# Kernel optimization log

Hardware: AMD Instinct MI355X
Metric: run time of the kernel (lower is better)

The kernel has to match this reference:

```python
import jax, jax.numpy as jnp
import numpy as np

B, S, I, H = 64, 512, 512, 1024

def setup_inputs() -> dict:
    key = jax.random.key(0)
    k1, k2, k3, k4, k5 = jax.random.split(key, 5)
    bound = 1.0 / np.sqrt(H)  # PyTorch RNNCell init scale (values only; distribution irrelevant for correctness)
    return {
        "x_in": jax.random.normal(k1, (B, S, I), dtype=jnp.float32),
        "W_ih": jax.random.uniform(k2, (H, I), dtype=jnp.float32, minval=-bound, maxval=bound),
        "W_hh": jax.random.uniform(k3, (H, H), dtype=jnp.float32, minval=-bound, maxval=bound),
        "b_ih": jax.random.uniform(k4, (H,), dtype=jnp.float32, minval=-bound, maxval=bound),
        "b_hh": jax.random.uniform(k5, (H,), dtype=jnp.float32, minval=-bound, maxval=bound),
    }

def reference(x_in, W_ih, W_hh, b_ih, b_hh):
    # batch_first=True: x_in is (B, S, I). Permute to time-major (S, B, I).
    x_tm = jnp.transpose(x_in, (1, 0, 2))
    # Precompute input projections for all timesteps in one big GEMM: (S, B, H)
    x_proj = jnp.einsum("sbi,hi->sbh", x_tm, W_ih) + b_ih + b_hh
    h0 = jnp.zeros((x_in.shape[0], W_hh.shape[0]), dtype=x_in.dtype)

    def step(h, xp_t):
        h_new = jnp.tanh(xp_t + h @ W_hh.T)
        return h_new, h_new

    _, hiddens = jax.lax.scan(step, h0, x_proj)  # (S, B, H)
    return jnp.transpose(hiddens, (1, 0, 2))  # back to (B, S, H)
```

## Files before the change

kernel.cpp:

```cpp
#include <hip/hip_runtime.h>
#include <hip/hip_bf16.h>
#include <math.h>

#define B_ 64
#define S_ 512
#define I_ 512
#define H_ 1024

typedef __attribute__((ext_vector_type(8))) short short8;
typedef __attribute__((ext_vector_type(4))) short short4v;
typedef __attribute__((ext_vector_type(4))) float f32x4;

__device__ inline short bf16bits(float f) {
    __hip_bfloat16 h = __float2bfloat16(f);
    return __builtin_bit_cast(short, h);
}

#define BM 128
#define BN 128
#define BK 32
#define LDT 40

__global__ __launch_bounds__(256) void xproj_gemm(const float* __restrict__ X,
                                                  const float* __restrict__ Wih,
                                                  const float* __restrict__ bih,
                                                  const float* __restrict__ bhh,
                                                  float* __restrict__ out) {
    __shared__ __hip_bfloat16 sA[BM * LDT];
    __shared__ __hip_bfloat16 sB[BN * LDT];
    const int tid  = threadIdx.x;
    const int m0   = blockIdx.x * BM;
    const int n0   = blockIdx.y * BN;
    const int wave = tid >> 6;
    const int lane = tid & 63;
    const int quad = lane >> 4;
    const int l16  = lane & 15;
    const int wm   = (wave >> 1) * 64;
    const int wn   = (wave & 1) * 64;

    f32x4 acc[4][4] = {};

    for (int k0 = 0; k0 < I_; k0 += BK) {
#pragma unroll
        for (int i = 0; i < 4; ++i) {
            int idx = tid + i * 256;
            int r   = idx >> 3;
            int c4  = idx & 7;
            f32x4 a = *reinterpret_cast<const f32x4*>(X   + (size_t)(m0 + r) * I_ + k0 + c4 * 4);
            f32x4 b = *reinterpret_cast<const f32x4*>(Wih + (size_t)(n0 + r) * I_ + k0 + c4 * 4);
            short4v ap, bp;
            ap[0] = bf16bits(a[0]); ap[1] = bf16bits(a[1]); ap[2] = bf16bits(a[2]); ap[3] = bf16bits(a[3]);
            bp[0] = bf16bits(b[0]); bp[1] = bf16bits(b[1]); bp[2] = bf16bits(b[2]); bp[3] = bf16bits(b[3]);
            int off = r * LDT + c4 * 4;
            *reinterpret_cast<short4v*>(&sA[off]) = ap;
            *reinterpret_cast<short4v*>(&sB[off]) = bp;
        }
        __syncthreads();

        short8 af[4], bf[4];
#pragma unroll
        for (int mt = 0; mt < 4; ++mt)
            af[mt] = *reinterpret_cast<const short8*>(&sA[(wm + mt * 16 + l16) * LDT + quad * 8]);
#pragma unroll
        for (int nt = 0; nt < 4; ++nt)
            bf[nt] = *reinterpret_cast<const short8*>(&sB[(wn + nt * 16 + l16) * LDT + quad * 8]);
#pragma unroll
        for (int mt = 0; mt < 4; ++mt)
#pragma unroll
            for (int nt = 0; nt < 4; ++nt)
                acc[mt][nt] = __builtin_amdgcn_mfma_f32_16x16x32_bf16(af[mt], bf[nt], acc[mt][nt], 0, 0, 0);
        __syncthreads();
    }

#pragma unroll
    for (int mt = 0; mt < 4; ++mt) {
#pragma unroll
        for (int nt = 0; nt < 4; ++nt) {
            int gm = m0 + wm + mt * 16 + quad * 4;
            int gn = n0 + wn + nt * 16 + l16;
            float bias = bih[gn] + bhh[gn];
#pragma unroll
            for (int r = 0; r < 4; ++r)
                out[(size_t)(gm + r) * H_ + gn] = acc[mt][nt][r] + bias;
        }
    }
}

#define WLD 1032

__global__ __launch_bounds__(256) void rnn_steps(const float* __restrict__ Whh,
                                                 float* __restrict__ out,
                                                 unsigned short* __restrict__ hbuf,
                                                 unsigned int* __restrict__ cnt) {
    __shared__ __hip_bfloat16 Wl[16 * WLD];
    __shared__ float red[4][16][17];
    const int tid  = threadIdx.x;
    const int bid  = blockIdx.x;
    const int g    = bid >> 6;
    const int jblk = bid & 63;
    const int j0   = jblk * 16;
    const int b0   = g * 16;
    const int wave = tid >> 6;
    const int lane = tid & 63;
    const int quad = lane >> 4;
    const int l16  = lane & 15;
    const int m    = tid >> 4;
    const int n    = tid & 15;

    for (int idx = tid; idx < 16 * 256; idx += 256) {
        int r  = idx >> 8;
        int c4 = idx & 255;
        f32x4 w = *reinterpret_cast<const f32x4*>(Whh + (size_t)(j0 + r) * H_ + c4 * 4);
        short4v wp;
        wp[0] = bf16bits(w[0]); wp[1] = bf16bits(w[1]); wp[2] = bf16bits(w[2]); wp[3] = bf16bits(w[3]);
        *reinterpret_cast<short4v*>(&Wl[r * WLD + c4 * 4]) = wp;
    }
    __syncthreads();

    const size_t orow = (size_t)(b0 + m) * S_ * H_ + (j0 + n);
    unsigned int* mycnt = cnt + g * 32;

    for (int t = 0; t < S_; ++t) {
        float xp = __builtin_nontemporal_load(out + orow + (size_t)t * H_);
        float s = 0.f;

        if (t > 0) {
            if (tid == 0) {
                const unsigned int target = (unsigned int)t * 64u;
                int guard = 0;
                while (__hip_atomic_load(mycnt, __ATOMIC_RELAXED, __HIP_MEMORY_SCOPE_AGENT) < target) {
                    __builtin_amdgcn_s_sleep(1);
                    if (++guard > 1000000) break;
                }
                (void)__hip_atomic_load(mycnt, __ATOMIC_ACQUIRE, __HIP_MEMORY_SCOPE_AGENT);
            }
            __syncthreads();

            const unsigned short* hprev = hbuf + (size_t)((t - 1) & 1) * (B_ * H_);
            f32x4 acc = {0.f, 0.f, 0.f, 0.f};
            const int kbase = wave * 256;
#pragma unroll
            for (int i = 0; i < 8; ++i) {
                int k = kbase + i * 32 + quad * 8;
                short8 av = *reinterpret_cast<const short8*>(hprev + (size_t)(b0 + l16) * H_ + k);
                short8 bv = *reinterpret_cast<const short8*>(&Wl[l16 * WLD + k]);
                acc = __builtin_amdgcn_mfma_f32_16x16x32_bf16(av, bv, acc, 0, 0, 0);
            }
#pragma unroll
            for (int r = 0; r < 4; ++r)
                red[wave][quad * 4 + r][l16] = acc[r];
            __syncthreads();

            s = red[0][m][n] + red[1][m][n] + red[2][m][n] + red[3][m][n];
        }

        float val = tanhf(xp + s);
        __builtin_nontemporal_store(val, out + orow + (size_t)t * H_);

        float nb = __shfl_xor(val, 1, 64);
        unsigned int pair = ((unsigned int)(unsigned short)bf16bits(nb) << 16)
                          | (unsigned int)(unsigned short)bf16bits(val);
        if ((n & 1) == 0) {
            unsigned int* dst = (unsigned int*)(hbuf + (size_t)(t & 1) * (B_ * H_)
                                                + (size_t)(b0 + m) * H_ + (j0 + n));
            __hip_atomic_store(dst, pair, __ATOMIC_RELAXED, __HIP_MEMORY_SCOPE_AGENT);
        }
        __syncthreads();

        if (t < S_ - 1 && tid == 0) {
            __hip_atomic_fetch_add(mycnt, 1u, __ATOMIC_RELAXED, __HIP_MEMORY_SCOPE_AGENT);
        }
    }
}

extern "C" void kernel_launch(void* const* d_in, const int* in_sizes, int n_in,
                              void* d_out, int out_size, void* d_ws, size_t ws_size,
                              hipStream_t stream) {
    const float* x   = (const float*)d_in[0];
    const float* Wih = (const float*)d_in[1];
    const float* Whh = (const float*)d_in[2];
    const float* bih = (const float*)d_in[3];
    const float* bhh = (const float*)d_in[4];
    float* out = (float*)d_out;

    unsigned int* cnt = (unsigned int*)d_ws;
    unsigned short* hbuf = (unsigned short*)((char*)d_ws + 1024);

    hipMemsetAsync(d_ws, 0, 1024, stream);

    dim3 gA(256, 8);
    xproj_gemm<<<gA, 256, 0, stream>>>(x, Wih, bih, bhh, out);
    rnn_steps<<<256, 256, 0, stream>>>(Whh, out, hbuf, cnt);
}
```

Baseline: 2.336 ms.

## Replace counter barrier with per-element step-tagged hidden state flags in RNN kernel

The recurrent kernel is restructured so each block owns 4 batch rows by 64 hidden units instead of 16 by 16. The shared atomic step counter and its barrier are replaced by tagging every stored hidden value with its timestep in the upper 16 bits. Consumers poll the exact hidden words they need with cache-bypassing loads until the tags match, which removes the global counter round-trip and one block-wide sync per step. The cost is twice the hidden-buffer size, a larger workspace requirement with a fallback path, wasted MFMA rows (only 4 of 16 batch rows are real), and spin polling on global memory.

```diff
diff --git a/kernel.cpp b/kernel.cpp
--- a/kernel.cpp
+++ b/kernel.cpp
@@ -10,6 +10,7 @@
 typedef __attribute__((ext_vector_type(8))) short short8;
 typedef __attribute__((ext_vector_type(4))) short short4v;
 typedef __attribute__((ext_vector_type(4))) float f32x4;
+typedef __attribute__((ext_vector_type(4))) unsigned int u32x4;
 
 __device__ inline short bf16bits(float f) {
     __hip_bfloat16 h = __float2bfloat16(f);
@@ -86,12 +87,128 @@
     }
 }
 
+#define WLD2 1032
+
+__global__ __launch_bounds__(256) void rnn_steps_v4(const float* __restrict__ Whh,
+                                                    float* __restrict__ out,
+                                                    unsigned int* __restrict__ hbuf) {
+    __shared__ __hip_bfloat16 Wl[64 * WLD2];
+    __shared__ float red[2][4][4][65];
+    const int tid  = threadIdx.x;
+    const int bid  = blockIdx.x;
+    const int g    = bid >> 4;
+    const int jblk = bid & 15;
+    const int j0   = jblk * 64;
+    const int b0   = g * 4;
+    const int wave = tid >> 6;
+    const int lane = tid & 63;
+    const int quad = lane >> 4;
+    const int l16  = lane & 15;
+    const int m    = wave;
+    const int n    = lane;
+
+    for (int idx = tid; idx < 64 * 256; idx += 256) {
+        int r  = idx >> 8;
+        int c4 = idx & 255;
+        f32x4 w = *reinterpret_cast<const f32x4*>(Whh + (size_t)(j0 + r) * H_ + c4 * 4);
+        short4v wp;
+        wp[0] = bf16bits(w[0]); wp[1] = bf16bits(w[1]); wp[2] = bf16bits(w[2]); wp[3] = bf16bits(w[3]);
+        *reinterpret_cast<short4v*>(&Wl[r * WLD2 + c4 * 4]) = wp;
+    }
+    __syncthreads();
+
+    const size_t orow = (size_t)(b0 + m) * S_ * H_ + (j0 + n);
+    const int rb = b0 + (l16 & 3);
+    const int kw = wave * 256 + quad * 8;
+    unsigned int* const hp0 = hbuf + (size_t)rb * H_ + kw;
+    unsigned int* const hp1 = hp0 + (size_t)(B_ * H_);
+    unsigned int* const hst = hbuf + (size_t)(b0 + m) * H_ + (j0 + n);
+
+    for (int t = 0; t < S_; ++t) {
+        float xp = __builtin_nontemporal_load(out + orow + (size_t)t * H_);
+        float s = 0.f;
+        const int par = t & 1;
+
+        if (t > 0) {
+            unsigned int* hp = ((t - 1) & 1) ? hp1 : hp0;
+            const unsigned int target = (unsigned int)t;
+            u32x4 wa[8], wb[8];
+
+#pragma unroll
+            for (int f = 0; f < 8; ++f)
+                asm volatile("global_load_dwordx4 %0, %2, off sc0 sc1\n\t"
+                             "global_load_dwordx4 %1, %2, off offset:16 sc0 sc1"
+                             : "=&v"(wa[f]), "=&v"(wb[f]) : "v"(hp + f * 32) : "memory");
+            asm volatile("s_waitcnt vmcnt(0)" ::: "memory");
+            __builtin_amdgcn_sched_barrier(0);
+
+            bool okf[8];
+            int sweep = 0;
+            while (true) {
+                bool allok = true;
+#pragma unroll
+                for (int f = 0; f < 8; ++f) {
+                    bool ok = ((wa[f][0] >> 16) == target) & ((wa[f][1] >> 16) == target)
+                            & ((wa[f][2] >> 16) == target) & ((wa[f][3] >> 16) == target)
+                            & ((wb[f][0] >> 16) == target) & ((wb[f][1] >> 16) == target)
+                            & ((wb[f][2] >> 16) == target) & ((wb[f][3] >> 16) == target);
+                    okf[f] = (bool)__all((int)ok);
+                    allok = allok && okf[f];
+                }
+                if (allok) break;
+                if (++sweep > 16384) break;
+                __builtin_amdgcn_s_sleep(1);
+#pragma unroll
+                for (int f = 0; f < 8; ++f)
+                    if (!okf[f])
+                        asm volatile("global_load_dwordx4 %0, %2, off sc0 sc1\n\t"
+                                     "global_load_dwordx4 %1, %2, off offset:16 sc0 sc1"
+                                     : "=&v"(wa[f]), "=&v"(wb[f]) : "v"(hp + f * 32) : "memory");
+                asm volatile("s_waitcnt vmcnt(0)" ::: "memory");
+                __builtin_amdgcn_sched_barrier(0);
+            }
+
+            f32x4 acc[4] = {};
+#pragma unroll
+            for (int f = 0; f < 8; ++f) {
+                short8 av;
+                av[0] = (short)wa[f][0]; av[1] = (short)wa[f][1];
+                av[2] = (short)wa[f][2]; av[3] = (short)wa[f][3];
+                av[4] = (short)wb[f][0]; av[5] = (short)wb[f][1];
+                av[6] = (short)wb[f][2]; av[7] = (short)wb[f][3];
+#pragma unroll
+                for (int nt = 0; nt < 4; ++nt) {
+                    short8 bv = *reinterpret_cast<const short8*>(
+                        &Wl[(nt * 16 + l16) * WLD2 + kw + f * 32]);
+                    acc[nt] = __builtin_amdgcn_mfma_f32_16x16x32_bf16(av, bv, acc[nt], 0, 0, 0);
+                }
+            }
+            if (quad == 0) {
+#pragma unroll
+                for (int nt = 0; nt < 4; ++nt)
+#pragma unroll
+                    for (int r = 0; r < 4; ++r)
+                        red[par][wave][r][nt * 16 + l16] = acc[nt][r];
+            }
+            __syncthreads();
+            s = red[par][0][m][n] + red[par][1][m][n] + red[par][2][m][n] + red[par][3][m][n];
+        }
+
+        float val = tanhf(xp + s);
+        unsigned int word = ((unsigned int)(t + 1) << 16)
+                          | (unsigned int)(unsigned short)bf16bits(val);
+        __hip_atomic_store(hst + (size_t)par * (B_ * H_), word,
+                           __ATOMIC_RELAXED, __HIP_MEMORY_SCOPE_AGENT);
+        __builtin_nontemporal_store(val, out + orow + (size_t)t * H_);
+    }
+}
+
 #define WLD 1032
 
-__global__ __launch_bounds__(256) void rnn_steps(const float* __restrict__ Whh,
-                                                 float* __restrict__ out,
-                                                 unsigned short* __restrict__ hbuf,
-                                                 unsigned int* __restrict__ cnt) {
+__global__ __launch_bounds__(256) void rnn_steps_fb(const float* __restrict__ Whh,
+                                                    float* __restrict__ out,
+                                                    unsigned short* __restrict__ hbuf,
+                                                    unsigned int* __restrict__ cnt) {
     __shared__ __hip_bfloat16 Wl[16 * WLD];
     __shared__ float red[4][16][17];
     const int tid  = threadIdx.x;
@@ -183,12 +300,19 @@
     const float* bhh = (const float*)d_in[4];
     float* out = (float*)d_out;
 
-    unsigned int* cnt = (unsigned int*)d_ws;
-    unsigned short* hbuf = (unsigned short*)((char*)d_ws + 1024);
-
-    hipMemsetAsync(d_ws, 0, 1024, stream);
+    const size_t need_v4 = 1024 + (size_t)2 * B_ * H_ * 4;
 
     dim3 gA(256, 8);
-    xproj_gemm<<<gA, 256, 0, stream>>>(x, Wih, bih, bhh, out);
-    rnn_steps<<<256, 256, 0, stream>>>(Whh, out, hbuf, cnt);
-}
+    if (ws_size >= need_v4) {
+        hipMemsetAsync(d_ws, 0, need_v4, stream);
+        xproj_gemm<<<gA, 256, 0, stream>>>(x, Wih, bih, bhh, out);
+        unsigned int* hbuf = (unsigned int*)((char*)d_ws + 1024);
+        rnn_steps_v4<<<256, 256, 0, stream>>>(Whh, out, hbuf);
+    } else {
+        hipMemsetAsync(d_ws, 0, 1024, stream);
+        xproj_gemm<<<gA, 256, 0, stream>>>(x, Wih, bih, bhh, out);
+        unsigned int* cnt = (unsigned int*)d_ws;
+        unsigned short* hbuf = (unsigned short*)((char*)d_ws + 1024);
+        rnn_steps_fb<<<256, 256, 0, stream>>>(Whh, out, hbuf, cnt);
+    }
+}
```

Result: slower. 2.666 ms (+14.1%).
